# Kernel optimization log

Hardware: AMD Instinct MI355X
Metric: run time of the kernel (lower is better)

Reference implementation:

```python
import jax, jax.numpy as jnp
import numpy as np

N_NODES = 50000
N_EDGES = 1600000
N_GRAPHS = 1000


def setup_inputs() -> dict:
    key = jax.random.key(0)
    ks = jax.random.split(key, 16)
    s = 0.1
    return {
        "x": jax.random.normal(ks[0], (N_NODES, 7), jnp.float32),
        "edge_attr": jax.random.normal(ks[1], (N_EDGES, 4), jnp.float32),
        "edge_index": jax.random.randint(ks[2], (2, N_EDGES), 0, N_NODES),
        "batch": jnp.sort(jax.random.randint(ks[3], (N_NODES,), 0, N_GRAPHS)),
        "We1": jax.random.normal(ks[4], (4, 7), jnp.float32) * s,
        "be1": jnp.zeros((7,), jnp.float32),
        "W1a": jax.random.normal(ks[5], (7, 64), jnp.float32) * s,
        "b1a": jnp.zeros((64,), jnp.float32),
        "W1b": jax.random.normal(ks[6], (64, 64), jnp.float32) * s,
        "b1b": jnp.zeros((64,), jnp.float32),
        "We2": jax.random.normal(ks[7], (4, 64), jnp.float32) * s,
        "be2": jnp.zeros((64,), jnp.float32),
        "W2a": jax.random.normal(ks[8], (64, 64), jnp.float32) * s,
        "b2a": jnp.zeros((64,), jnp.float32),
        "W2b": jax.random.normal(ks[9], (64, 64), jnp.float32) * s,
        "b2b": jnp.zeros((64,), jnp.float32),
        "Wfc": jax.random.normal(ks[10], (64, 12), jnp.float32) * s,
        "bfc": jnp.zeros((12,), jnp.float32),
    }


def _gine_conv(h, edge_attr, src, dst, We, be, Wa, ba, Wb, bb, n_nodes):
    # GINEConv (eps=0): out = nn(h + sum_j relu(h[src] + lin(edge_attr)))
    e = edge_attr @ We + be                      # [E, d]
    msg = jax.nn.relu(h[src] + e)                # [E, d] gather + add + relu
    aggr = jax.ops.segment_sum(msg, dst, num_segments=n_nodes)  # scatter-sum
    z = h + aggr
    return jax.nn.relu(z @ Wa + ba) @ Wb + bb


def reference(x, edge_attr, edge_index, batch,
              We1, be1, W1a, b1a, W1b, b1b,
              We2, be2, W2a, b2a, W2b, b2b,
              Wfc, bfc):
    src, dst = edge_index[0], edge_index[1]
    n = x.shape[0]
    h = jax.nn.relu(_gine_conv(x, edge_attr, src, dst, We1, be1, W1a, b1a, W1b, b1b, n))
    h = jax.nn.relu(_gine_conv(h, edge_attr, src, dst, We2, be2, W2a, b2a, W2b, b2b, n))
    # global mean pool over batch index
    sums = jax.ops.segment_sum(h, batch, num_segments=N_GRAPHS)          # [G, 64]
    cnt = jax.ops.segment_sum(jnp.ones((n,), h.dtype), batch, num_segments=N_GRAPHS)
    pooled = sums / jnp.maximum(cnt, 1.0)[:, None]
    return pooled @ Wfc + bfc                                            # [G, 12]
```

## Files before the change

### kernel.cpp

```cpp
#include <hip/hip_runtime.h>

typedef unsigned char uchar;
typedef unsigned short ushort;
typedef unsigned int uint;

constexpr int NN = 50000;
constexpr int NE = 1600000;
constexpr int NG = 1000;
constexpr int NB2 = 196;
constexpr int TILE = 4096;
constexpr int NTILE = (NE + TILE - 1) / TILE;
constexpr int SPAN_CAP = 9216;
constexpr int MSTRIDE = 72;
constexpr int NPB = 16;
constexpr int NBLK2 = NN / NPB;

constexpr int OFF_BCNT  = 0;
constexpr int OFF_SUMS  = 256;
constexpr int OFF_CNT   = 64256;
constexpr int ZERO_UNITS= 65280;
constexpr int OFF_BBASE = 65280;
constexpr int OFF_BCUR  = 65536;
constexpr int OFF_OFFS  = 65792;
constexpr int OFF_P0    = 116224;
constexpr int OFF_P1    = 1716224;
constexpr int OFF_P2    = 3316224;
constexpr int OFF_Z1    = 4916224;
constexpr int OFF_H1    = 5316224;
constexpr int OFF_Z     = 6916224;

typedef __attribute__((ext_vector_type(8))) short short8;
typedef __attribute__((ext_vector_type(4))) float float4v;
typedef __attribute__((ext_vector_type(2))) float float2v;

__device__ __forceinline__ uint f2bf(float f) {
    uint u = __float_as_uint(f);
    return (u + 0x7fffu + ((u >> 16) & 1u)) >> 16;
}
__device__ __forceinline__ float bf2f_lo(uint p) { return __uint_as_float(p << 16); }
__device__ __forceinline__ float bf2f_hi(uint p) { return __uint_as_float(p & 0xffff0000u); }

__global__ __launch_bounds__(256) void bhist_kernel(const int* __restrict__ eidx,
                                                    int* __restrict__ bcnt) {
    __shared__ int lh[NB2];
    for (int i = threadIdx.x; i < NB2; i += 256) lh[i] = 0;
    __syncthreads();
    int tid = blockIdx.x * 256 + threadIdx.x;
    int stride = gridDim.x * 256;
    for (int e = tid; e < NE; e += stride) atomicAdd(&lh[eidx[NE + e] >> 8], 1);
    __syncthreads();
    for (int i = threadIdx.x; i < NB2; i += 256) if (lh[i]) atomicAdd(&bcnt[i], lh[i]);
}

__global__ __launch_bounds__(256) void bscan_kernel(const int* __restrict__ bcnt,
                                                    int* __restrict__ bbase,
                                                    int* __restrict__ bcur) {
    __shared__ int s[256];
    int t = threadIdx.x;
    int v = (t < NB2) ? bcnt[t] : 0;
    s[t] = v; __syncthreads();
    for (int o = 1; o < 256; o <<= 1) {
        int u = (t >= o) ? s[t - o] : 0;
        __syncthreads();
        s[t] += u;
        __syncthreads();
    }
    bbase[t] = s[t] - v;
    bcur[t] = s[t] - v;
}

__global__ __launch_bounds__(256) void bin_kernel(const int* __restrict__ eidx,
                                                  const float4* __restrict__ ea,
                                                  int* __restrict__ bcur,
                                                  uint* __restrict__ p0,
                                                  uint* __restrict__ p1,
                                                  uint* __restrict__ p2) {
    __shared__ uint s0[TILE], s1[TILE], s2[TILE];
    __shared__ int hcnt[NB2], hoff[NB2 + 1], hcur[NB2], gbase[NB2];
    const int t = threadIdx.x;
    const int e0 = blockIdx.x * TILE;
    const int cnt = (NE - e0 < TILE) ? (NE - e0) : TILE;
    for (int i = t; i < NB2; i += 256) hcnt[i] = 0;
    __syncthreads();
    int dsts[16];
    #pragma unroll
    for (int k = 0; k < 16; ++k) {
        int i = t + k * 256;
        int d = (i < cnt) ? eidx[NE + e0 + i] : -1;
        dsts[k] = d;
        if (d >= 0) atomicAdd(&hcnt[d >> 8], 1);
    }
    __syncthreads();
    if (t == 0) {
        int a = 0;
        for (int b = 0; b < NB2; ++b) { hoff[b] = a; a += hcnt[b]; }
        hoff[NB2] = a;
    }
    __syncthreads();
    if (t < NB2) { hcur[t] = hoff[t]; gbase[t] = atomicAdd(&bcur[t], hcnt[t]); }
    __syncthreads();
    #pragma unroll
    for (int k = 0; k < 16; ++k) {
        int d = dsts[k];
        if (d < 0) continue;
        int i = t + k * 256;
        int e = e0 + i;
        int src = eidx[e];
        float4 a = ea[e];
        int bkt = d >> 8;
        int lp = atomicAdd(&hcur[bkt], 1);
        s0[lp] = (uint)src | ((uint)(d & 255) << 16) | ((uint)bkt << 24);
        s1[lp] = f2bf(a.x) | (f2bf(a.y) << 16);
        s2[lp] = f2bf(a.z) | (f2bf(a.w) << 16);
    }
    __syncthreads();
    for (int i = t; i < cnt; i += 256) {
        uint r0 = s0[i];
        int bkt = (int)(r0 >> 24);
        int gp = gbase[bkt] + (i - hoff[bkt]);
        p0[gp] = r0; p1[gp] = s1[i]; p2[gp] = s2[i];
    }
}

__global__ __launch_bounds__(256) void build_kernel(const int* __restrict__ bbase,
                                                    const int* __restrict__ bcnt,
                                                    int* __restrict__ offs,
                                                    uint* __restrict__ p0,
                                                    uint* __restrict__ p1,
                                                    uint* __restrict__ p2) {
    __shared__ uint s0[SPAN_CAP], s1[SPAN_CAP], s2[SPAN_CAP];
    __shared__ int ldeg[256], lcur[256], sscan[256];
    const int t = threadIdx.x;
    const int b = blockIdx.x;
    const int nlo = b << 8;
    const int base = bbase[b];
    int span = bcnt[b];
    if (span > SPAN_CAP) span = SPAN_CAP;
    ldeg[t] = 0;
    __syncthreads();
    for (int i = t; i < span; i += 256)
        atomicAdd(&ldeg[(p0[base + i] >> 16) & 0xFFu], 1);
    __syncthreads();
    int v = ldeg[t];
    sscan[t] = v; __syncthreads();
    for (int o = 1; o < 256; o <<= 1) {
        int u = (t >= o) ? sscan[t - o] : 0;
        __syncthreads();
        sscan[t] += u;
        __syncthreads();
    }
    int exc = sscan[t] - v;
    lcur[t] = exc;
    int gi = nlo + t;
    if (gi < NN) offs[gi] = base + exc;
    else if (gi < 50176) offs[gi] = NE;
    __syncthreads();
    for (int i = t; i < span; i += 256) {
        uint r0 = p0[base + i], r1 = p1[base + i], r2 = p2[base + i];
        int pos = atomicAdd(&lcur[(r0 >> 16) & 0xFFu], 1);
        s0[pos] = r0; s1[pos] = r1; s2[pos] = r2;
    }
    __syncthreads();
    for (int i = t; i < span; i += 256) {
        p0[base + i] = s0[i]; p1[base + i] = s1[i]; p2[base + i] = s2[i];
    }
}

__global__ __launch_bounds__(256) void aggr1_kernel(
    const float* __restrict__ x,
    const uint* __restrict__ p0, const uint* __restrict__ p1, const uint* __restrict__ p2,
    const int* __restrict__ offs,
    const float* __restrict__ We1, const float* __restrict__ be1,
    float* __restrict__ z1)
{
    __shared__ float sWe[32];
    __shared__ float sbe[8];
    int tid = threadIdx.x;
    if (tid < 32) { int k = tid >> 3, dd = tid & 7; sWe[tid] = (dd < 7) ? We1[k * 7 + dd] : 0.f; }
    if (tid < 8)  sbe[tid] = (tid < 7) ? be1[tid] : 0.f;
    __syncthreads();

    const int w = tid >> 6, lane = tid & 63;
    const int jg = lane >> 3, d = lane & 7;

    for (int n = blockIdx.x * 4 + w; n < NN; n += gridDim.x * 4) {
        const int off = offs[n];
        const int deg = offs[n + 1] - off;
        float acc = 0.f;
        for (int j0 = 0; j0 < deg; j0 += 16) {
            int ja = j0 + jg;
            int jb = j0 + 8 + jg;
            int ia = off + ((ja < deg) ? ja : 0);
            int ib = off + ((jb < deg) ? jb : 0);
            uint r0a = p0[ia], r1a = p1[ia], r2a = p2[ia];
            uint r0b = p0[ib], r1b = p1[ib], r2b = p2[ib];
            float xa = (d < 7) ? x[(size_t)(r0a & 0xFFFFu) * 7 + d] : 0.f;
            float xb = (d < 7) ? x[(size_t)(r0b & 0xFFFFu) * 7 + d] : 0.f;
            float va = sbe[d] + bf2f_lo(r1a) * sWe[d] + bf2f_hi(r1a) * sWe[8 + d]
                     + bf2f_lo(r2a) * sWe[16 + d] + bf2f_hi(r2a) * sWe[24 + d] + xa;
            float vb = sbe[d] + bf2f_lo(r1b) * sWe[d] + bf2f_hi(r1b) * sWe[8 + d]
                     + bf2f_lo(r2b) * sWe[16 + d] + bf2f_hi(r2b) * sWe[24 + d] + xb;
            va = (d < 7 && ja < deg) ? fmaxf(va, 0.f) : 0.f;
            vb = (d < 7 && jb < deg) ? fmaxf(vb, 0.f) : 0.f;
            acc += va + vb;
        }
        acc += __shfl_xor(acc, 8);
        acc += __shfl_xor(acc, 16);
        acc += __shfl_xor(acc, 32);
        if (jg == 0)
            z1[(size_t)n * 8 + d] = (d < 7) ? (x[(size_t)n * 7 + d] + acc) : 0.f;
    }
}

__global__ __launch_bounds__(256) void node1_kernel(
    const float* __restrict__ z1,
    const float* __restrict__ W1a, const float* __restrict__ b1a,
    const float* __restrict__ W1b, const float* __restrict__ b1b,
    uint* __restrict__ h1u)
{
    __shared__ __align__(16) ushort sT[64 * MSTRIDE];
    __shared__ __align__(16) ushort sO[64 * 64];
    const int t = threadIdx.x;
    const int w = t >> 6, lane = t & 63;
    const int qm = lane & 15, quad = lane >> 4;
    const int n0 = blockIdx.x * 64;
    const int node = n0 + w * 16 + qm;

    short8 wa1n[4];
    #pragma unroll
    for (int nt = 0; nt < 4; ++nt) {
        short8 v = (short8)0;
        if (quad == 0) {
            #pragma unroll
            for (int j = 0; j < 7; ++j)
                v[j] = (short)f2bf(W1a[j * 64 + nt * 16 + qm]);
        }
        wa1n[nt] = v;
    }
    short8 wb1[2][4];
    #pragma unroll
    for (int s = 0; s < 2; ++s)
        #pragma unroll
        for (int nt = 0; nt < 4; ++nt) {
            short8 v;
            #pragma unroll
            for (int j = 0; j < 8; ++j)
                v[j] = (short)f2bf(W1b[(s * 32 + quad * 8 + j) * 64 + nt * 16 + qm]);
            wb1[s][nt] = v;
        }
    float ba[4], bb[4];
    #pragma unroll
    for (int nt = 0; nt < 4; ++nt) { ba[nt] = b1a[nt * 16 + qm]; bb[nt] = b1b[nt * 16 + qm]; }

    short8 af1 = (short8)0;
    if (quad == 0 && node < NN) {
        const float4 za = *(const float4*)(z1 + (size_t)node * 8);
        const float4 zbv = *(const float4*)(z1 + (size_t)node * 8 + 4);
        af1[0] = (short)f2bf(za.x); af1[1] = (short)f2bf(za.y);
        af1[2] = (short)f2bf(za.z); af1[3] = (short)f2bf(za.w);
        af1[4] = (short)f2bf(zbv.x); af1[5] = (short)f2bf(zbv.y);
        af1[6] = (short)f2bf(zbv.z); af1[7] = (short)f2bf(zbv.w);
    }
    float4v acc[4];
    #pragma unroll
    for (int nt = 0; nt < 4; ++nt) {
        acc[nt] = (float4v){0.f, 0.f, 0.f, 0.f};
        acc[nt] = __builtin_amdgcn_mfma_f32_16x16x32_bf16(af1, wa1n[nt], acc[nt], 0, 0, 0);
    }
    #pragma unroll
    for (int nt = 0; nt < 4; ++nt)
        #pragma unroll
        for (int r = 0; r < 4; ++r)
            sT[(w * 16 + quad * 4 + r) * MSTRIDE + nt * 16 + qm] =
                (ushort)f2bf(fmaxf(acc[nt][r] + ba[nt], 0.f));
    __syncthreads();

    #pragma unroll
    for (int nt = 0; nt < 4; ++nt) acc[nt] = (float4v){0.f, 0.f, 0.f, 0.f};
    #pragma unroll
    for (int s = 0; s < 2; ++s) {
        short8 af = *(const short8*)&sT[(w * 16 + qm) * MSTRIDE + s * 32 + quad * 8];
        #pragma unroll
        for (int nt = 0; nt < 4; ++nt)
            acc[nt] = __builtin_amdgcn_mfma_f32_16x16x32_bf16(af, wb1[s][nt], acc[nt], 0, 0, 0);
    }
    #pragma unroll
    for (int nt = 0; nt < 4; ++nt)
        #pragma unroll
        for (int r = 0; r < 4; ++r)
            sO[(w * 16 + quad * 4 + r) * 64 + nt * 16 + qm] =
                (ushort)f2bf(fmaxf(acc[nt][r] + bb[nt], 0.f));
    __syncthreads();
    for (int i = t; i < 64 * 32; i += 256) {
        int nd = i >> 5;
        if (n0 + nd < NN) h1u[(size_t)(n0 + nd) * 32 + (i & 31)] = ((const uint*)sO)[i];
    }
}

__global__ __launch_bounds__(256) void aggr2_kernel(
    const uint* __restrict__ h1u,
    const uint* __restrict__ p0, const uint* __restrict__ p1, const uint* __restrict__ p2,
    const int* __restrict__ offs,
    const float* __restrict__ We2, const float* __restrict__ be2,
    uint* __restrict__ zb)
{
    const int tid = threadIdx.x;
    const int lane = tid & 63;
    const int wv = tid >> 6;
    const int grp = lane >> 4;
    const int cl = lane & 15;
    const int n = blockIdx.x * NPB + wv * 4 + grp;

    float2v wA[4], wB[4], bA, bB;
    #pragma unroll
    for (int k = 0; k < 4; ++k) {
        const float4 w4 = *(const float4*)&We2[k * 64 + 4 * cl];
        wA[k][0] = w4.x; wA[k][1] = w4.y;
        wB[k][0] = w4.z; wB[k][1] = w4.w;
    }
    {
        const float4 b4 = *(const float4*)&be2[4 * cl];
        bA[0] = b4.x; bA[1] = b4.y;
        bB[0] = b4.z; bB[1] = b4.w;
    }

    const int off = offs[n];
    const int deg = offs[n + 1] - off;
    const int degm1 = (deg > 0) ? deg - 1 : 0;
    const int offC = (deg > 0) ? off : 0;
    int dmax = deg;
    dmax = max(dmax, __shfl_xor(dmax, 16));
    dmax = max(dmax, __shfl_xor(dmax, 32));

    float2v accA = {0.f, 0.f}, accB = {0.f, 0.f};
    const float2v zero2 = {0.f, 0.f};
    int j = 0;
    for (; j + 2 <= dmax; j += 2) {
        const bool q0 = (j < deg), q1 = (j + 1 < deg);
        const int e0 = offC + (q0 ? j : degm1);
        const int e1 = offC + (q1 ? j + 1 : degm1);
        const uint r00 = p0[e0], ry0 = p1[e0], rz0 = p2[e0];
        const uint r01 = p0[e1], ry1 = p1[e1], rz1 = p2[e1];
        const uint2 g0 = *(const uint2*)&h1u[((size_t)(r00 & 0xFFFFu) << 5) + 2 * cl];
        const uint2 g1 = *(const uint2*)&h1u[((size_t)(r01 & 0xFFFFu) << 5) + 2 * cl];
        {
            float2v bvA = bA + bf2f_lo(ry0) * wA[0] + bf2f_hi(ry0) * wA[1]
                        + bf2f_lo(rz0) * wA[2] + bf2f_hi(rz0) * wA[3];
            float2v bvB = bB + bf2f_lo(ry0) * wB[0] + bf2f_hi(ry0) * wB[1]
                        + bf2f_lo(rz0) * wB[2] + bf2f_hi(rz0) * wB[3];
            float2v tA, tB;
            tA[0] = fmaxf(bf2f_lo(g0.x) + bvA[0], 0.f);
            tA[1] = fmaxf(bf2f_hi(g0.x) + bvA[1], 0.f);
            tB[0] = fmaxf(bf2f_lo(g0.y) + bvB[0], 0.f);
            tB[1] = fmaxf(bf2f_hi(g0.y) + bvB[1], 0.f);
            accA += q0 ? tA : zero2;
            accB += q0 ? tB : zero2;
        }
        {
            float2v bvA = bA + bf2f_lo(ry1) * wA[0] + bf2f_hi(ry1) * wA[1]
                        + bf2f_lo(rz1) * wA[2] + bf2f_hi(rz1) * wA[3];
            float2v bvB = bB + bf2f_lo(ry1) * wB[0] + bf2f_hi(ry1) * wB[1]
                        + bf2f_lo(rz1) * wB[2] + bf2f_hi(rz1) * wB[3];
            float2v tA, tB;
            tA[0] = fmaxf(bf2f_lo(g1.x) + bvA[0], 0.f);
            tA[1] = fmaxf(bf2f_hi(g1.x) + bvA[1], 0.f);
            tB[0] = fmaxf(bf2f_lo(g1.y) + bvB[0], 0.f);
            tB[1] = fmaxf(bf2f_hi(g1.y) + bvB[1], 0.f);
            accA += q1 ? tA : zero2;
            accB += q1 ? tB : zero2;
        }
    }
    if (j < dmax) {
        const bool q0 = (j < deg);
        const int e0 = offC + (q0 ? j : degm1);
        const uint r00 = p0[e0], ry0 = p1[e0], rz0 = p2[e0];
        const uint2 g0 = *(const uint2*)&h1u[((size_t)(r00 & 0xFFFFu) << 5) + 2 * cl];
        float2v bvA = bA + bf2f_lo(ry0) * wA[0] + bf2f_hi(ry0) * wA[1]
                    + bf2f_lo(rz0) * wA[2] + bf2f_hi(rz0) * wA[3];
        float2v bvB = bB + bf2f_lo(ry0) * wB[0] + bf2f_hi(ry0) * wB[1]
                    + bf2f_lo(rz0) * wB[2] + bf2f_hi(rz0) * wB[3];
        float2v tA, tB;
        tA[0] = fmaxf(bf2f_lo(g0.x) + bvA[0], 0.f);
        tA[1] = fmaxf(bf2f_hi(g0.x) + bvA[1], 0.f);
        tB[0] = fmaxf(bf2f_lo(g0.y) + bvB[0], 0.f);
        tB[1] = fmaxf(bf2f_hi(g0.y) + bvB[1], 0.f);
        accA += q0 ? tA : zero2;
        accB += q0 ? tB : zero2;
    }

    const uint2 hw = *(const uint2*)&h1u[(size_t)n * 32 + 2 * cl];
    uint o0 = f2bf(bf2f_lo(hw.x) + accA[0]) | (f2bf(bf2f_hi(hw.x) + accA[1]) << 16);
    uint o1 = f2bf(bf2f_lo(hw.y) + accB[0]) | (f2bf(bf2f_hi(hw.y) + accB[1]) << 16);
    uint2 ov; ov.x = o0; ov.y = o1;
    *(uint2*)&zb[(size_t)n * 32 + 2 * cl] = ov;
}

__global__ __launch_bounds__(256) void mlp2_kernel(
    const uint* __restrict__ zb,
    const float* __restrict__ W2a, const float* __restrict__ b2a,
    const float* __restrict__ W2b, const float* __restrict__ b2b,
    const int* __restrict__ batch,
    float* __restrict__ sums, float* __restrict__ cnt)
{
    __shared__ __align__(16) ushort sT[64 * MSTRIDE];
    __shared__ float sH[64 * 64];
    __shared__ int sB[64];
    __shared__ float pbuf[4][64];
    __shared__ int pcnt[4];
    const int t = threadIdx.x;
    const int w = t >> 6, lane = t & 63;
    const int qm = lane & 15, quad = lane >> 4;
    const int n0 = blockIdx.x * 64;
    const int node = n0 + w * 16 + qm;
    const int nv = (NN - n0 < 64) ? (NN - n0) : 64;

    if (t < 64) sB[t] = (n0 + t < NN) ? batch[n0 + t] : -2;

    short8 wa[2][4], wb[2][4];
    #pragma unroll
    for (int s = 0; s < 2; ++s)
        #pragma unroll
        for (int nt = 0; nt < 4; ++nt) {
            short8 va, vb;
            #pragma unroll
            for (int j = 0; j < 8; ++j) {
                int k = s * 32 + quad * 8 + j, n = nt * 16 + qm;
                va[j] = (short)f2bf(W2a[k * 64 + n]);
                vb[j] = (short)f2bf(W2b[k * 64 + n]);
            }
            wa[s][nt] = va; wb[s][nt] = vb;
        }
    float ba[4], bb[4];
    #pragma unroll
    for (int nt = 0; nt < 4; ++nt) { ba[nt] = b2a[nt * 16 + qm]; bb[nt] = b2b[nt * 16 + qm]; }

    float4v acc[4];
    #pragma unroll
    for (int nt = 0; nt < 4; ++nt) acc[nt] = (float4v){0.f, 0.f, 0.f, 0.f};
    #pragma unroll
    for (int s = 0; s < 2; ++s) {
        uint4 zw = (node < NN) ? *(const uint4*)&zb[(size_t)node * 32 + s * 16 + quad * 4]
                               : make_uint4(0, 0, 0, 0);
        short8 af;
        *(uint4*)&af = zw;
        #pragma unroll
        for (int nt = 0; nt < 4; ++nt)
            acc[nt] = __builtin_amdgcn_mfma_f32_16x16x32_bf16(af, wa[s][nt], acc[nt], 0, 0, 0);
    }
    #pragma unroll
    for (int nt = 0; nt < 4; ++nt)
        #pragma unroll
        for (int r = 0; r < 4; ++r)
            sT[(w * 16 + quad * 4 + r) * MSTRIDE + nt * 16 + qm] =
                (ushort)f2bf(fmaxf(acc[nt][r] + ba[nt], 0.f));
    __syncthreads();

    #pragma unroll
    for (int nt = 0; nt < 4; ++nt) acc[nt] = (float4v){0.f, 0.f, 0.f, 0.f};
    #pragma unroll
    for (int s = 0; s < 2; ++s) {
        short8 af = *(const short8*)&sT[(w * 16 + qm) * MSTRIDE + s * 32 + quad * 8];
        #pragma unroll
        for (int nt = 0; nt < 4; ++nt)
            acc[nt] = __builtin_amdgcn_mfma_f32_16x16x32_bf16(af, wb[s][nt], acc[nt], 0, 0, 0);
    }
    #pragma unroll
    for (int nt = 0; nt < 4; ++nt)
        #pragma unroll
        for (int r = 0; r < 4; ++r)
            sH[(w * 16 + quad * 4 + r) * 64 + nt * 16 + qm] = fmaxf(acc[nt][r] + bb[nt], 0.f);
    __syncthreads();

    const int glo = sB[0];
    const int ghi = sB[nv - 1];
    const int c = t >> 6, d = t & 63;
    for (int g = glo; g <= ghi; ++g) {
        float p = 0.f;
        int lc = 0;
        #pragma unroll 4
        for (int i = 0; i < 16; ++i) {
            int nd = c * 16 + i;
            if (sB[nd] == g) { p += sH[nd * 64 + d]; ++lc; }
        }
        pbuf[c][d] = p;
        if (d == 0) pcnt[c] = lc;
        __syncthreads();
        int tc = pcnt[0] + pcnt[1] + pcnt[2] + pcnt[3];
        if (tc > 0) {
            if (c == 0) {
                float tot = pbuf[0][d] + pbuf[1][d] + pbuf[2][d] + pbuf[3][d];
                atomicAdd(&sums[(size_t)g * 64 + d], tot);
            }
            if (t == 0) atomicAdd(&cnt[g], (float)tc);
        }
        __syncthreads();
    }
}

__global__ __launch_bounds__(256) void fc_kernel(
    const float* __restrict__ sums, const float* __restrict__ cnt,
    const float* __restrict__ Wfc, const float* __restrict__ bfc,
    float* __restrict__ out)
{
    int gid = blockIdx.x * blockDim.x + threadIdx.x;
    if (gid >= NG * 12) return;
    int g = gid / 12, jj = gid - g * 12;
    float inv = 1.f / fmaxf(cnt[g], 1.f);
    float acc = bfc[jj];
    #pragma unroll 8
    for (int k = 0; k < 64; ++k) acc += sums[(size_t)g * 64 + k] * inv * Wfc[k * 12 + jj];
    out[gid] = acc;
}

extern "C" void kernel_launch(void* const* d_in, const int* in_sizes, int n_in,
                              void* d_out, int out_size, void* d_ws, size_t ws_size,
                              hipStream_t stream)
{
    (void)in_sizes; (void)n_in; (void)out_size; (void)ws_size;
    const float*  x    = (const float*)d_in[0];
    const float4* ea   = (const float4*)d_in[1];
    const int*    eidx = (const int*)d_in[2];
    const int*    batch= (const int*)d_in[3];
    const float*  We1  = (const float*)d_in[4];
    const float*  be1  = (const float*)d_in[5];
    const float*  W1a  = (const float*)d_in[6];
    const float*  b1a  = (const float*)d_in[7];
    const float*  W1b  = (const float*)d_in[8];
    const float*  b1b  = (const float*)d_in[9];
    const float*  We2  = (const float*)d_in[10];
    const float*  be2  = (const float*)d_in[11];
    const float*  W2a  = (const float*)d_in[12];
    const float*  b2a  = (const float*)d_in[13];
    const float*  W2b  = (const float*)d_in[14];
    const float*  b2b  = (const float*)d_in[15];
    const float*  Wfc  = (const float*)d_in[16];
    const float*  bfc  = (const float*)d_in[17];
    float* out = (float*)d_out;
    float* ws  = (float*)d_ws;

    int*   bcnt  = (int*)(ws + OFF_BCNT);
    float* sums  = ws + OFF_SUMS;
    float* cnt   = ws + OFF_CNT;
    int*   bbase = (int*)(ws + OFF_BBASE);
    int*   bcur  = (int*)(ws + OFF_BCUR);
    int*   offs  = (int*)(ws + OFF_OFFS);
    uint*  p0    = (uint*)(ws + OFF_P0);
    uint*  p1    = (uint*)(ws + OFF_P1);
    uint*  p2    = (uint*)(ws + OFF_P2);
    float* z1    = ws + OFF_Z1;
    uint*  h1u   = (uint*)(ws + OFF_H1);
    uint*  zb    = (uint*)(ws + OFF_Z);

    hipMemsetAsync(d_ws, 0, (size_t)ZERO_UNITS * 4, stream);

    bhist_kernel<<<256, 256, 0, stream>>>(eidx, bcnt);
    bscan_kernel<<<1, 256, 0, stream>>>(bcnt, bbase, bcur);
    bin_kernel  <<<NTILE, 256, 0, stream>>>(eidx, ea, bcur, p0, p1, p2);
    build_kernel<<<NB2, 256, 0, stream>>>(bbase, bcnt, offs, p0, p1, p2);
    aggr1_kernel<<<2500, 256, 0, stream>>>(x, p0, p1, p2, offs, We1, be1, z1);
    node1_kernel<<<(NN + 63) / 64, 256, 0, stream>>>(z1, W1a, b1a, W1b, b1b, h1u);
    aggr2_kernel<<<NBLK2, 256, 0, stream>>>(h1u, p0, p1, p2, offs, We2, be2, zb);
    mlp2_kernel <<<(NN + 63) / 64, 256, 0, stream>>>(zb, W2a, b2a, W2b, b2b, batch, sums, cnt);
    fc_kernel   <<<(NG * 12 + 255) / 256, 256, 0, stream>>>(sums, cnt, Wfc, bfc, out);
}
```

Baseline: 275.1 us.

## Remap first-layer aggregation to four lanes per node over padded x

```diff
diff --git a/kernel.cpp b/kernel.cpp
--- a/kernel.cpp
+++ b/kernel.cpp
@@ -166,49 +166,94 @@
     }
 }
 
+__global__ __launch_bounds__(256) void xpack_kernel(const float* __restrict__ x,
+                                                    float* __restrict__ xp) {
+    int i = blockIdx.x * 256 + threadIdx.x;
+    if (i < NN * 8) {
+        int n = i >> 3, c = i & 7;
+        xp[i] = (c < 7) ? x[n * 7 + c] : 0.f;
+    }
+}
+
 __global__ __launch_bounds__(256) void aggr1_kernel(
-    const float* __restrict__ x,
+    const float* __restrict__ xp,
     const uint* __restrict__ p0, const uint* __restrict__ p1, const uint* __restrict__ p2,
     const int* __restrict__ offs,
     const float* __restrict__ We1, const float* __restrict__ be1,
     float* __restrict__ z1)
 {
-    __shared__ float sWe[32];
-    __shared__ float sbe[8];
-    int tid = threadIdx.x;
-    if (tid < 32) { int k = tid >> 3, dd = tid & 7; sWe[tid] = (dd < 7) ? We1[k * 7 + dd] : 0.f; }
-    if (tid < 8)  sbe[tid] = (tid < 7) ? be1[tid] : 0.f;
-    __syncthreads();
-
-    const int w = tid >> 6, lane = tid & 63;
-    const int jg = lane >> 3, d = lane & 7;
-
-    for (int n = blockIdx.x * 4 + w; n < NN; n += gridDim.x * 4) {
-        const int off = offs[n];
-        const int deg = offs[n + 1] - off;
-        float acc = 0.f;
-        for (int j0 = 0; j0 < deg; j0 += 16) {
-            int ja = j0 + jg;
-            int jb = j0 + 8 + jg;
-            int ia = off + ((ja < deg) ? ja : 0);
-            int ib = off + ((jb < deg) ? jb : 0);
-            uint r0a = p0[ia], r1a = p1[ia], r2a = p2[ia];
-            uint r0b = p0[ib], r1b = p1[ib], r2b = p2[ib];
-            float xa = (d < 7) ? x[(size_t)(r0a & 0xFFFFu) * 7 + d] : 0.f;
-            float xb = (d < 7) ? x[(size_t)(r0b & 0xFFFFu) * 7 + d] : 0.f;
-            float va = sbe[d] + bf2f_lo(r1a) * sWe[d] + bf2f_hi(r1a) * sWe[8 + d]
-                     + bf2f_lo(r2a) * sWe[16 + d] + bf2f_hi(r2a) * sWe[24 + d] + xa;
-            float vb = sbe[d] + bf2f_lo(r1b) * sWe[d] + bf2f_hi(r1b) * sWe[8 + d]
-                     + bf2f_lo(r2b) * sWe[16 + d] + bf2f_hi(r2b) * sWe[24 + d] + xb;
-            va = (d < 7 && ja < deg) ? fmaxf(va, 0.f) : 0.f;
-            vb = (d < 7 && jb < deg) ? fmaxf(vb, 0.f) : 0.f;
-            acc += va + vb;
-        }
-        acc += __shfl_xor(acc, 8);
-        acc += __shfl_xor(acc, 16);
-        acc += __shfl_xor(acc, 32);
-        if (jg == 0)
-            z1[(size_t)n * 8 + d] = (d < 7) ? (x[(size_t)n * 7 + d] + acc) : 0.f;
+    const int tid = threadIdx.x;
+    const int lane = tid & 63;
+    const int wv = tid >> 6;
+    const int grp = lane >> 2;
+    const int cl = lane & 3;
+    const int n = blockIdx.x * 64 + wv * 16 + grp;
+
+    float2v wE[4], bE;
+    const bool c1ok = (2 * cl + 1 < 7);
+    #pragma unroll
+    for (int k = 0; k < 4; ++k) {
+        wE[k][0] = We1[k * 7 + 2 * cl];
+        wE[k][1] = c1ok ? We1[k * 7 + 2 * cl + 1] : 0.f;
+    }
+    bE[0] = be1[2 * cl];
+    bE[1] = c1ok ? be1[2 * cl + 1] : 0.f;
+
+    const int off = offs[n];
+    const int deg = offs[n + 1] - off;
+    const int degm1 = (deg > 0) ? deg - 1 : 0;
+    const int offC = (deg > 0) ? off : 0;
+    int dmax = deg;
+    dmax = max(dmax, __shfl_xor(dmax, 4));
+    dmax = max(dmax, __shfl_xor(dmax, 8));
+    dmax = max(dmax, __shfl_xor(dmax, 16));
+    dmax = max(dmax, __shfl_xor(dmax, 32));
+
+    float2v acc = {0.f, 0.f};
+    const float2v zero2 = {0.f, 0.f};
+    int j = 0;
+    for (; j + 2 <= dmax; j += 2) {
+        const bool q0 = (j < deg), q1 = (j + 1 < deg);
+        const int e0 = offC + (q0 ? j : degm1);
+        const int e1 = offC + (q1 ? j + 1 : degm1);
+        const uint r00 = p0[e0], ry0 = p1[e0], rz0 = p2[e0];
+        const uint r01 = p0[e1], ry1 = p1[e1], rz1 = p2[e1];
+        const float2v xg0 = *(const float2v*)&xp[((size_t)(r00 & 0xFFFFu) << 3) + 2 * cl];
+        const float2v xg1 = *(const float2v*)&xp[((size_t)(r01 & 0xFFFFu) << 3) + 2 * cl];
+        {
+            float2v ev = bE + bf2f_lo(ry0) * wE[0] + bf2f_hi(ry0) * wE[1]
+                       + bf2f_lo(rz0) * wE[2] + bf2f_hi(rz0) * wE[3];
+            float2v tv = xg0 + ev;
+            tv[0] = fmaxf(tv[0], 0.f);
+            tv[1] = fmaxf(tv[1], 0.f);
+            acc += q0 ? tv : zero2;
+        }
+        {
+            float2v ev = bE + bf2f_lo(ry1) * wE[0] + bf2f_hi(ry1) * wE[1]
+                       + bf2f_lo(rz1) * wE[2] + bf2f_hi(rz1) * wE[3];
+            float2v tv = xg1 + ev;
+            tv[0] = fmaxf(tv[0], 0.f);
+            tv[1] = fmaxf(tv[1], 0.f);
+            acc += q1 ? tv : zero2;
+        }
+    }
+    if (j < dmax) {
+        const bool q0 = (j < deg);
+        const int e0 = offC + (q0 ? j : degm1);
+        const uint r00 = p0[e0], ry0 = p1[e0], rz0 = p2[e0];
+        const float2v xg0 = *(const float2v*)&xp[((size_t)(r00 & 0xFFFFu) << 3) + 2 * cl];
+        float2v ev = bE + bf2f_lo(ry0) * wE[0] + bf2f_hi(ry0) * wE[1]
+                   + bf2f_lo(rz0) * wE[2] + bf2f_hi(rz0) * wE[3];
+        float2v tv = xg0 + ev;
+        tv[0] = fmaxf(tv[0], 0.f);
+        tv[1] = fmaxf(tv[1], 0.f);
+        acc += q0 ? tv : zero2;
+    }
+
+    if (n < NN) {
+        const float2v xn = *(const float2v*)&xp[(size_t)n * 8 + 2 * cl];
+        float2v zv = xn + acc;
+        *(float2v*)&z1[(size_t)n * 8 + 2 * cl] = zv;
     }
 }
 
@@ -550,6 +595,7 @@
     float* z1    = ws + OFF_Z1;
     uint*  h1u   = (uint*)(ws + OFF_H1);
     uint*  zb    = (uint*)(ws + OFF_Z);
+    float* xp    = ws + OFF_Z;
 
     hipMemsetAsync(d_ws, 0, (size_t)ZERO_UNITS * 4, stream);
 
@@ -557,7 +603,8 @@
     bscan_kernel<<<1, 256, 0, stream>>>(bcnt, bbase, bcur);
     bin_kernel  <<<NTILE, 256, 0, stream>>>(eidx, ea, bcur, p0, p1, p2);
     build_kernel<<<NB2, 256, 0, stream>>>(bbase, bcnt, offs, p0, p1, p2);
-    aggr1_kernel<<<2500, 256, 0, stream>>>(x, p0, p1, p2, offs, We1, be1, z1);
+    xpack_kernel<<<(NN * 8 + 255) / 256, 256, 0, stream>>>(x, xp);
+    aggr1_kernel<<<(NN + 63) / 64, 256, 0, stream>>>(xp, p0, p1, p2, offs, We1, be1, z1);
     node1_kernel<<<(NN + 63) / 64, 256, 0, stream>>>(z1, W1a, b1a, W1b, b1b, h1u);
     aggr2_kernel<<<NBLK2, 256, 0, stream>>>(h1u, p0, p1, p2, offs, We2, be2, zb);
     mlp2_kernel <<<(NN + 63) / 64, 256, 0, stream>>>(zb, W2a, b2a, W2b, b2b, batch, sums, cnt);
```

New measurement: 294.0 us. 6.8% more time.
